# Performance work log

Measured on AMD Instinct MI355X. Metric: run time of the kernel, lower is better.

## Reference

```python
import jax, jax.numpy as jnp
import numpy as np

D_MODEL = 1024
N_HEADS = 16
D_HEAD = D_MODEL // N_HEADS
D_FF = 4096
ACT_BITS = 8
GSIZE = 64
EPS = 1e-6


def act_quant(x):
    # per-group int8 activation quantization with straight-through estimator
    qmax = 2.0 ** (ACT_BITS - 1) - 1.0  # 127
    g = x.reshape(x.shape[:-1] + (-1, GSIZE))
    s = jnp.clip(jnp.max(jnp.abs(g), axis=-1, keepdims=True), 1e-5, None) / qmax
    q = jnp.clip(jnp.round(g / s), -qmax, qmax) * s
    out = g + jax.lax.stop_gradient(q - g)  # STE
    return out.reshape(x.shape)


def weight_quant_1b(w):
    # binarize to sign(w) * mean(|w|), STE
    alpha = jnp.mean(jnp.abs(w))
    wq = jnp.sign(w) * alpha
    return w + jax.lax.stop_gradient(wq - w)


def bitlinear(x, w):
    # y = Q_act(x) @ Q_w(w)^T ; w is [out, in]
    return act_quant(x) @ weight_quant_1b(w).T


def rmsnorm(x, g):
    return x * jax.lax.rsqrt(jnp.mean(x * x, axis=-1, keepdims=True) + EPS) * g


def causal_sdpa(q, k, v):
    # q,k,v: [B,H,T,Dh]
    T = q.shape[2]
    scores = jnp.einsum('bhqd,bhkd->bhqk', q, k) / jnp.sqrt(jnp.asarray(D_HEAD, q.dtype))
    mask = jnp.tril(jnp.ones((T, T), dtype=bool))
    scores = jnp.where(mask, scores, jnp.asarray(-1e30, q.dtype))
    p = jax.nn.softmax(scores, axis=-1)
    return jnp.einsum('bhqk,bhkd->bhqd', p, v)


def setup_inputs() -> dict:
    key = jax.random.key(0)
    ks = jax.random.split(key, 11)
    sd = 0.02
    inp = {
        'x': jax.random.normal(ks[0], (1, 4096, D_MODEL), dtype=jnp.float32),
        'wq': jax.random.normal(ks[1], (D_MODEL, D_MODEL), dtype=jnp.float32) * sd,
        'wk': jax.random.normal(ks[2], (D_MODEL, D_MODEL), dtype=jnp.float32) * sd,
        'wv': jax.random.normal(ks[3], (D_MODEL, D_MODEL), dtype=jnp.float32) * sd,
        'wo': jax.random.normal(ks[4], (D_MODEL, D_MODEL), dtype=jnp.float32) * sd,
        'w1': jax.random.normal(ks[5], (D_FF, D_MODEL), dtype=jnp.float32) * sd,
        'w2': jax.random.normal(ks[6], (D_FF, D_MODEL), dtype=jnp.float32) * sd,
        'w3': jax.random.normal(ks[7], (D_MODEL, D_FF), dtype=jnp.float32) * sd,
        'g1': jnp.ones((D_MODEL,), dtype=jnp.float32),
        'g2': jnp.ones((D_MODEL,), dtype=jnp.float32),
    }
    return inp


def reference(x, wq, wk, wv, wo, w1, w2, w3, g1, g2):
    B, T, C = x.shape
    # attention branch
    h = rmsnorm(x, g1)
    q = bitlinear(h, wq).reshape(B, T, N_HEADS, D_HEAD).transpose(0, 2, 1, 3)
    k = bitlinear(h, wk).reshape(B, T, N_HEADS, D_HEAD).transpose(0, 2, 1, 3)
    v = bitlinear(h, wv).reshape(B, T, N_HEADS, D_HEAD).transpose(0, 2, 1, 3)
    y = causal_sdpa(q, k, v).transpose(0, 2, 1, 3).reshape(B, T, C)
    x = x + bitlinear(y, wo)
    # SwiGLU FFN branch
    h2 = rmsnorm(x, g2)
    ff = bitlinear(jax.nn.silu(bitlinear(h2, w1)) * bitlinear(h2, w2), w3)
    return x + ff
```

## Files before the change

### kernel.cpp

```cpp
#include <hip/hip_runtime.h>
#include <math.h>


typedef unsigned short u16;
typedef unsigned int u32;
typedef __attribute__((ext_vector_type(2))) unsigned int u32x2;
typedef __attribute__((ext_vector_type(4))) float f32x4;
typedef __attribute__((ext_vector_type(4))) unsigned short u16x4;
typedef __attribute__((ext_vector_type(8))) unsigned short u16x8;
typedef __attribute__((ext_vector_type(8))) __bf16 bf16x8;

#define DEV static __device__ __forceinline__

DEV float bf2f(u16 u) { union { unsigned i; float f; } c; c.i = ((unsigned)u) << 16; return c.f; }
DEV u16 f2bf(float f) { __bf16 b = (__bf16)f; return __builtin_bit_cast(u16, b); }
DEV float fexp2(float x) { float r; asm("v_exp_f32 %0, %1" : "=v"(r) : "v"(x)); return r; }
DEV u32 cvtpk(float lo, float hi) {
  u32 r; asm("v_cvt_pk_bf16_f32 %0, %1, %2" : "=v"(r) : "v"(lo), "v"(hi)); return r;
}

DEV void gload16(const void* g, void* l) {
  __builtin_amdgcn_global_load_lds((__attribute__((address_space(1))) void*)g,
                                   (__attribute__((address_space(3))) void*)l,
                                   16, 0, 0);
}

__global__ __launch_bounds__(256) void convert_sign_all(
    const float* __restrict__ w0, const float* __restrict__ w1,
    const float* __restrict__ w2, const float* __restrict__ w3,
    const float* __restrict__ w4, const float* __restrict__ w5,
    const float* __restrict__ w6, u16* __restrict__ sgn_base,
    float* __restrict__ partial,
    const float* __restrict__ x, const float* __restrict__ g1,
    u16* __restrict__ hq) {
  __shared__ float red[4];
  const int wi = blockIdx.y;
  const int t = threadIdx.x;

  if (wi == 7) {
#pragma unroll 1
    for (int rr = 0; rr < 16; ++rr) {
      const int row = blockIdx.x * 16 + rr;
      f32x4 v = ((const f32x4*)(x + (size_t)row * 1024))[t];
      float ss = v[0] * v[0] + v[1] * v[1] + v[2] * v[2] + v[3] * v[3];
#pragma unroll
      for (int off = 32; off >= 1; off >>= 1) ss += __shfl_xor(ss, off);
      if ((t & 63) == 0) red[t >> 6] = ss;
      __syncthreads();
      float tot = red[0] + red[1] + red[2] + red[3];
      __syncthreads();
      float rinv = rsqrtf(tot * (1.f / 1024.f) + 1e-6f);
      f32x4 gg = ((const f32x4*)g1)[t];
      float n[4];
#pragma unroll
      for (int j = 0; j < 4; ++j) n[j] = v[j] * rinv * gg[j];
      float gm = fmaxf(fmaxf(fabsf(n[0]), fabsf(n[1])), fmaxf(fabsf(n[2]), fabsf(n[3])));
#pragma unroll
      for (int off = 1; off <= 8; off <<= 1) gm = fmaxf(gm, __shfl_xor(gm, off));
      float s = fmaxf(gm, 1e-5f) / 127.0f;
      u16x4 o;
#pragma unroll
      for (int j = 0; j < 4; ++j) {
        float q = fminf(fmaxf(rintf(n[j] / s), -127.f), 127.f) * s;
        o[j] = f2bf(q);
      }
      ((u16x4*)hq)[(size_t)row * 256 + t] = o;
    }
    return;
  }

  const float* srcs[7] = {w0, w1, w2, w3, w4, w5, w6};
  const size_t offs[7] = {0, 1048576, 2097152, 3145728, 4194304, 4194304, 12582912};
  const float* w = srcs[wi];
  u16* sgn = sgn_base + offs[wi];
  const int n4 = (wi < 4) ? 262144 : 1048576;
  const bool ilv = (wi == 4) || (wi == 5);
  const int ilv_add = (wi == 5) ? 16 : 0;

  float s = 0.f;
  for (int i = blockIdx.x * 256 + t; i < n4; i += 256 * 256) {
    f32x4 v = ((const f32x4*)w)[i];
    u16x4 o;
#pragma unroll
    for (int j = 0; j < 4; ++j) {
      float f = v[j];
      o[j] = f > 0.f ? (u16)0x3F80 : (f < 0.f ? (u16)0xBF80 : (u16)0);
      s += fabsf(f);
    }
    size_t di = i;
    if (ilv) {
      int e = i << 2;
      int row = e >> 10, col = e & 1023;
      int dst = ((row >> 4) << 5) + ilv_add + (row & 15);
      di = ((size_t)dst << 8) + (col >> 2);
    }
    ((u16x4*)sgn)[di] = o;
  }
#pragma unroll
  for (int off = 32; off >= 1; off >>= 1) s += __shfl_xor(s, off);
  if ((t & 63) == 0) red[t >> 6] = s;
  __syncthreads();
  if (t == 0)
    partial[wi * 256 + blockIdx.x] = red[0] + red[1] + red[2] + red[3];
}

__global__ __launch_bounds__(256) void finalize_alpha(
    const float* __restrict__ partial, float* __restrict__ alphas) {
  __shared__ float red[4];
  int wi = blockIdx.x;
  float v = partial[wi * 256 + threadIdx.x];
#pragma unroll
  for (int off = 32; off >= 1; off >>= 1) v += __shfl_xor(v, off);
  if ((threadIdx.x & 63) == 0) red[threadIdx.x >> 6] = v;
  __syncthreads();
  if (threadIdx.x == 0)
    alphas[wi] = (red[0] + red[1] + red[2] + red[3]) *
                 (wi < 4 ? (1.f / 1048576.f) : (1.f / 4194304.f));
}

__global__ __launch_bounds__(256) void rmsnorm_quant(
    const float* __restrict__ x, const float* __restrict__ g, u16* __restrict__ out) {
  __shared__ float red[4];
  const int row = blockIdx.x, t = threadIdx.x;
  f32x4 v = ((const f32x4*)(x + (size_t)row * 1024))[t];
  float ss = v[0] * v[0] + v[1] * v[1] + v[2] * v[2] + v[3] * v[3];
#pragma unroll
  for (int off = 32; off >= 1; off >>= 1) ss += __shfl_xor(ss, off);
  if ((t & 63) == 0) red[t >> 6] = ss;
  __syncthreads();
  float tot = red[0] + red[1] + red[2] + red[3];
  float rinv = rsqrtf(tot * (1.f / 1024.f) + 1e-6f);
  f32x4 gg = ((const f32x4*)g)[t];
  float n[4];
#pragma unroll
  for (int j = 0; j < 4; ++j) n[j] = v[j] * rinv * gg[j];
  float gm = fmaxf(fmaxf(fabsf(n[0]), fabsf(n[1])), fmaxf(fabsf(n[2]), fabsf(n[3])));
#pragma unroll
  for (int off = 1; off <= 8; off <<= 1) gm = fmaxf(gm, __shfl_xor(gm, off));
  float s = fmaxf(gm, 1e-5f) / 127.0f;
  u16x4 o;
#pragma unroll
  for (int j = 0; j < 4; ++j) {
    float q = fminf(fmaxf(rintf(n[j] / s), -127.f), 127.f) * s;
    o[j] = f2bf(q);
  }
  ((u16x4*)out)[(size_t)row * 256 + t] = o;
}

__global__ __launch_bounds__(256) void transpose_v(
    const u16* __restrict__ qkv, u16* __restrict__ Vt) {
  __shared__ u16 T[64][65];
  const int tt = blockIdx.x, h = blockIdx.y, tid = threadIdx.x;
#pragma unroll
  for (int i = 0; i < 2; ++i) {
    int idx = i * 2048 + tid * 8;
    int trow = idx >> 6, dcol = idx & 63;
    u16x8 v = *(const u16x8*)(qkv + (size_t)(tt * 64 + trow) * 3072 + 2048 + h * 64 + dcol);
#pragma unroll
    for (int j = 0; j < 8; ++j) T[dcol + j][trow] = v[j];
  }
  __syncthreads();
#pragma unroll
  for (int i = 0; i < 2; ++i) {
    int idx = i * 2048 + tid * 8;
    int drow = idx >> 6, tcol = idx & 63;
    u16x8 v;
#pragma unroll
    for (int j = 0; j < 8; ++j) v[j] = T[drow][tcol + j];
    *(u16x8*)(Vt + ((size_t)h * 64 + drow) * 4096 + tt * 64 + tcol) = v;
  }
}

template <bool RES, int BM>
__global__ __launch_bounds__(256) void gemm_bt(
    const u16* __restrict__ A, const u16* __restrict__ B,
    const float* __restrict__ alpha, int ashift, const float* __restrict__ res,
    void* __restrict__ Cout, int M, int N, int K) {
  constexpr int NI = (BM == 128) ? 4 : 2;
  constexpr int WNE = (BM == 128) ? 64 : 32;
  __shared__ u16 As[BM * 64];
  __shared__ u16 Bs[128 * 64];
  const int tid = threadIdx.x;
  const int l = tid & 63, w = tid >> 6;
  const int wm = (BM == 128) ? (w >> 1) : 0;
  const int wn = (BM == 128) ? (w & 1) : w;
  const int lr = l & 15, lg = l >> 4;
  const int xorv = (l & 7) << 4;
  const int brow = blockIdx.y * BM;
  const int bcol = blockIdx.x * 128;
  const int src_chunk = (l & 7) ^ (l >> 3);
  const int rl = w * 8 + (l >> 3);

  f32x4 acc[4][NI];
#pragma unroll
  for (int i = 0; i < 4; ++i)
#pragma unroll
    for (int j = 0; j < NI; ++j) acc[i][j] = (f32x4){0.f, 0.f, 0.f, 0.f};

  const char* Ag = (const char*)A;
  const char* Bg = (const char*)B;
  const int nkt = K >> 6;
  for (int kt = 0; kt < nkt; ++kt) {
    __syncthreads();
    const size_t kb = (size_t)kt * 128 + src_chunk * 16;
#pragma unroll
    for (int it = 0; it < BM / 32; ++it)
      gload16(Ag + (size_t)(brow + it * 32 + rl) * (size_t)(K * 2) + kb,
              &As[(it * 32 + w * 8) * 64]);
#pragma unroll
    for (int it = 0; it < 4; ++it)
      gload16(Bg + (size_t)(bcol + it * 32 + rl) * (size_t)(K * 2) + kb,
              &Bs[(it * 32 + w * 8) * 64]);
    __syncthreads();

    bf16x8 af[4][2], bfr[NI][2];
#pragma unroll
    for (int mi = 0; mi < 4; ++mi)
#pragma unroll
      for (int ks = 0; ks < 2; ++ks) {
        int row = wm * 64 + mi * 16 + lr;
        af[mi][ks] = *(const bf16x8*)((const char*)As + row * 128 + ((ks * 64 + lg * 16) ^ xorv));
      }
#pragma unroll
    for (int ni = 0; ni < NI; ++ni)
#pragma unroll
      for (int ks = 0; ks < 2; ++ks) {
        int row = wn * WNE + ni * 16 + lr;
        bfr[ni][ks] = *(const bf16x8*)((const char*)Bs + row * 128 + ((ks * 64 + lg * 16) ^ xorv));
      }
#pragma unroll
    for (int ks = 0; ks < 2; ++ks)
#pragma unroll
      for (int mi = 0; mi < 4; ++mi)
#pragma unroll
        for (int ni = 0; ni < NI; ++ni)
          acc[mi][ni] = __builtin_amdgcn_mfma_f32_16x16x32_bf16(
              af[mi][ks], bfr[ni][ks], acc[mi][ni], 0, 0, 0);
  }

  const float scale = alpha[bcol >> ashift];
#pragma unroll
  for (int mi = 0; mi < 4; ++mi)
#pragma unroll
    for (int ni = 0; ni < NI; ++ni)
#pragma unroll
      for (int r = 0; r < 4; ++r) {
        int row = brow + wm * 64 + mi * 16 + lg * 4 + r;
        int col = bcol + wn * WNE + ni * 16 + lr;
        float vv = acc[mi][ni][r] * scale;
        if (RES)
          ((float*)Cout)[(size_t)row * N + col] = res[(size_t)row * N + col] + vv;
        else
          ((u16*)Cout)[(size_t)row * N + col] = f2bf(vv);
      }
}

template <bool RES>
__global__ __launch_bounds__(256, 2) void gemm_fat(
    const u16* __restrict__ A, const u16* __restrict__ B,
    const float* __restrict__ alpha, int ashift, const float* __restrict__ res,
    void* __restrict__ Cout, int M, int N, int K) {
  __shared__ u16 As[256 * 64];
  __shared__ u16 Bs[128 * 64];
  const int tid = threadIdx.x;
  const int l = tid & 63, w = tid >> 6;
  const int wm = w >> 1, wn = w & 1;
  const int lr = l & 15, lg = l >> 4;
  const int xorv = (l & 7) << 4;
  const int brow = blockIdx.y * 256;
  const int bcol = blockIdx.x * 128;
  const int src_chunk = (l & 7) ^ (l >> 3);
  const int rl = w * 8 + (l >> 3);

  f32x4 acc[8][4];
#pragma unroll
  for (int i = 0; i < 8; ++i)
#pragma unroll
    for (int j = 0; j < 4; ++j) acc[i][j] = (f32x4){0.f, 0.f, 0.f, 0.f};

  const int nkt = K >> 6;
  for (int kt = 0; kt < nkt; ++kt) {
    __syncthreads();
    const size_t kb = (size_t)kt * 128 + src_chunk * 16;
#pragma unroll
    for (int it = 0; it < 8; ++it)
      gload16((const char*)A + (size_t)(brow + it * 32 + rl) * (size_t)(K * 2) + kb,
              &As[(it * 32 + w * 8) * 64]);
#pragma unroll
    for (int it = 0; it < 4; ++it)
      gload16((const char*)B + (size_t)(bcol + it * 32 + rl) * (size_t)(K * 2) + kb,
              &Bs[(it * 32 + w * 8) * 64]);
    __syncthreads();

#pragma unroll
    for (int ks = 0; ks < 2; ++ks) {
      bf16x8 bfr[4];
#pragma unroll
      for (int ni = 0; ni < 4; ++ni)
        bfr[ni] = *(const bf16x8*)((const char*)Bs + (wn * 64 + ni * 16 + lr) * 128 +
                                   ((ks * 64 + lg * 16) ^ xorv));
#pragma unroll
      for (int mi = 0; mi < 8; ++mi) {
        bf16x8 af = *(const bf16x8*)((const char*)As + (wm * 128 + mi * 16 + lr) * 128 +
                                     ((ks * 64 + lg * 16) ^ xorv));
#pragma unroll
        for (int ni = 0; ni < 4; ++ni)
          acc[mi][ni] = __builtin_amdgcn_mfma_f32_16x16x32_bf16(
              af, bfr[ni], acc[mi][ni], 0, 0, 0);
      }
    }
  }

  const float scale = alpha[bcol >> ashift];
#pragma unroll
  for (int mi = 0; mi < 8; ++mi)
#pragma unroll
    for (int ni = 0; ni < 4; ++ni)
#pragma unroll
      for (int r = 0; r < 4; ++r) {
        int row = brow + wm * 128 + mi * 16 + lg * 4 + r;
        int col = bcol + wn * 64 + ni * 16 + lr;
        float vv = acc[mi][ni][r] * scale;
        if (RES)
          ((float*)Cout)[(size_t)row * N + col] = res[(size_t)row * N + col] + vv;
        else
          ((u16*)Cout)[(size_t)row * N + col] = f2bf(vv);
      }
}

__global__ __launch_bounds__(256, 2) void gemm_ffn(
    const u16* __restrict__ A, const u16* __restrict__ B12,
    const float* __restrict__ alpha2, u16* __restrict__ zq) {
  __shared__ u16 As[256 * 64];
  __shared__ u16 Bs[128 * 64];
  const int tid = threadIdx.x;
  const int l = tid & 63, w = tid >> 6;
  const int wm = w >> 1, wn = w & 1;
  const int lr = l & 15, lg = l >> 4;
  const int xorv = (l & 7) << 4;
  const int brow = blockIdx.y * 256;
  const int bcol = blockIdx.x * 128;
  const int src_chunk = (l & 7) ^ (l >> 3);
  const int rl = w * 8 + (l >> 3);

  f32x4 acc[8][4];
#pragma unroll
  for (int i = 0; i < 8; ++i)
#pragma unroll
    for (int j = 0; j < 4; ++j) acc[i][j] = (f32x4){0.f, 0.f, 0.f, 0.f};

  for (int kt = 0; kt < 16; ++kt) {
    __syncthreads();
    const size_t kb = (size_t)kt * 128 + src_chunk * 16;
#pragma unroll
    for (int it = 0; it < 8; ++it)
      gload16((const char*)A + (size_t)(brow + it * 32 + rl) * 2048 + kb,
              &As[(it * 32 + w * 8) * 64]);
#pragma unroll
    for (int it = 0; it < 4; ++it)
      gload16((const char*)B12 + (size_t)(bcol + it * 32 + rl) * 2048 + kb,
              &Bs[(it * 32 + w * 8) * 64]);
    __syncthreads();

#pragma unroll
    for (int ks = 0; ks < 2; ++ks) {
      bf16x8 bfr[4];
#pragma unroll
      for (int ni = 0; ni < 4; ++ni)
        bfr[ni] = *(const bf16x8*)((const char*)Bs + (wn * 64 + ni * 16 + lr) * 128 +
                                   ((ks * 64 + lg * 16) ^ xorv));
#pragma unroll
      for (int mi = 0; mi < 8; ++mi) {
        bf16x8 af = *(const bf16x8*)((const char*)As + (wm * 128 + mi * 16 + lr) * 128 +
                                     ((ks * 64 + lg * 16) ^ xorv));
#pragma unroll
        for (int ni = 0; ni < 4; ++ni)
          acc[mi][ni] = __builtin_amdgcn_mfma_f32_16x16x32_bf16(
              af, bfr[ni], acc[mi][ni], 0, 0, 0);
      }
    }
  }

  const float a1 = alpha2[0], a2 = alpha2[1];
  const float L2E = 1.4426950408889634f;
  float zl[8][4], zh[8][4], rm[8][4];
#pragma unroll
  for (int mi = 0; mi < 8; ++mi)
#pragma unroll
    for (int r = 0; r < 4; ++r) {
      float y1 = acc[mi][0][r] * a1;
      zl[mi][r] = y1 / (1.f + fexp2(-L2E * y1)) * (acc[mi][1][r] * a2);
      float y3 = acc[mi][2][r] * a1;
      zh[mi][r] = y3 / (1.f + fexp2(-L2E * y3)) * (acc[mi][3][r] * a2);
      float g = fmaxf(fabsf(zl[mi][r]), fabsf(zh[mi][r]));
#pragma unroll
      for (int off = 1; off <= 8; off <<= 1) g = fmaxf(g, __shfl_xor(g, off));
      rm[mi][r] = g;
    }

  float* rmax = (float*)&As[0];
  __syncthreads();
  if (lr == 0) {
#pragma unroll
    for (int mi = 0; mi < 8; ++mi)
#pragma unroll
      for (int r = 0; r < 4; ++r)
        rmax[w * 128 + mi * 16 + lg * 4 + r] = rm[mi][r];
  }
  __syncthreads();

#pragma unroll
  for (int mi = 0; mi < 8; ++mi)
#pragma unroll
    for (int r = 0; r < 4; ++r) {
      float g = fmaxf(rm[mi][r], rmax[(w ^ 1) * 128 + mi * 16 + lg * 4 + r]);
      float gmc = fmaxf(g, 1e-5f);
      float s = gmc * (1.f / 127.f);
      float inv = 127.f / gmc;
      int row = brow + wm * 128 + mi * 16 + lg * 4 + r;
      int zc = blockIdx.x * 64 + wn * 32 + lr;
      float q0 = fminf(fmaxf(rintf(zl[mi][r] * inv), -127.f), 127.f) * s;
      float q1 = fminf(fmaxf(rintf(zh[mi][r] * inv), -127.f), 127.f) * s;
      zq[(size_t)row * 4096 + zc] = f2bf(q0);
      zq[(size_t)row * 4096 + zc + 16] = f2bf(q1);
    }
}

__global__ __launch_bounds__(512) void attn_kernel(
    const u16* __restrict__ QKV, const u16* __restrict__ Vt, u16* __restrict__ Y) {
  __shared__ u16 Ks[2][64 * 64];
  __shared__ u16 Vs[2][64 * 64];
  __shared__ u16 Ps[8][16 * 64];

  const int tid = threadIdx.x;
  const int l = tid & 63, w = tid >> 6;
  const int lr = l & 15, lg = l >> 4;
  const int xorv = (l & 7) << 4;
  const int h = blockIdx.x;
  const int y = blockIdx.y;
  const int qt = (y < 16) ? y : (47 - y);
  const int src_chunk = (l & 7) ^ (l >> 3);
  const int rl = w * 8 + (l >> 3);
  const float SC = 0.18033688f;

  const int qrow0 = qt * 128 + w * 16;
  const int nkt = 2 * qt + 2;

  bf16x8 qf[2];
#pragma unroll
  for (int ks = 0; ks < 2; ++ks)
    qf[ks] = __builtin_bit_cast(
        bf16x8, *(const u16x8*)(QKV + (size_t)(qrow0 + lr) * 3072 +
                                h * 64 + ks * 32 + lg * 8));

  f32x4 O[4];
#pragma unroll
  for (int ni = 0; ni < 4; ++ni) O[ni] = (f32x4){0.f, 0.f, 0.f, 0.f};
  float m_ = -3e38f, lsum = 0.f;

  auto STAGE = [&](int buf, int kt) {
    int krow = kt * 64 + rl;
    gload16((const char*)QKV + ((size_t)krow * 3072 + 1024 + h * 64) * 2 + src_chunk * 16,
            &Ks[buf][(w * 8) * 64]);
    gload16((const char*)Vt + (((size_t)h * 64 + rl) * 4096 + kt * 64) * 2 + src_chunk * 16,
            &Vs[buf][(w * 8) * 64]);
  };

  STAGE(0, 0);
#pragma unroll 1
  for (int kt = 0; kt < nkt; ++kt) {
    const int cur = kt & 1;
    if (kt + 1 < nkt) {
      STAGE(cur ^ 1, kt + 1);
      asm volatile("s_waitcnt vmcnt(2)" ::: "memory");
    } else {
      asm volatile("s_waitcnt vmcnt(0)" ::: "memory");
    }
    __builtin_amdgcn_s_barrier();
    __builtin_amdgcn_sched_barrier(0);

    const char* kbase = (const char*)&Ks[cur][0];
    const char* vbase = (const char*)&Vs[cur][0];

    f32x4 S[4];
    __builtin_amdgcn_s_setprio(1);
#pragma unroll
    for (int ni = 0; ni < 4; ++ni) {
      S[ni] = (f32x4){0.f, 0.f, 0.f, 0.f};
#pragma unroll
      for (int ks = 0; ks < 2; ++ks) {
        bf16x8 kf = *(const bf16x8*)(kbase + (ni * 16 + lr) * 128 +
                                     ((ks * 64 + lg * 16) ^ xorv));
        S[ni] = __builtin_amdgcn_mfma_f32_16x16x32_bf16(kf, qf[ks], S[ni], 0, 0, 0);
      }
    }
    __builtin_amdgcn_s_setprio(0);

    const int tb = kt * 64;
    if (tb + 63 > qrow0) {
#pragma unroll
      for (int ni = 0; ni < 4; ++ni)
#pragma unroll
        for (int r = 0; r < 4; ++r)
          if (tb + ni * 16 + lg * 4 + r > qrow0 + lr) S[ni][r] = -3e38f;
    }

    float nm = -3e38f;
#pragma unroll
    for (int ni = 0; ni < 4; ++ni)
#pragma unroll
      for (int r = 0; r < 4; ++r) nm = fmaxf(nm, S[ni][r]);
    nm = fmaxf(nm, __shfl_xor(nm, 16));
    nm = fmaxf(nm, __shfl_xor(nm, 32));
    float nms = nm * SC;
    if (__ballot(nms > m_ + 8.f)) {
      float mn = fmaxf(m_, nms);
      float fac = fexp2(m_ - mn);
      m_ = mn;
      lsum *= fac;
#pragma unroll
      for (int ni = 0; ni < 4; ++ni) O[ni] *= fac;
    }
    float rs = 0.f;
#pragma unroll
    for (int ni = 0; ni < 4; ++ni)
#pragma unroll
      for (int r = 0; r < 4; ++r) {
        float pv = fexp2(__builtin_fmaf(S[ni][r], SC, -m_));
        S[ni][r] = pv;
        rs += pv;
      }
    rs += __shfl_xor(rs, 16);
    rs += __shfl_xor(rs, 32);
    lsum += rs;

#pragma unroll
    for (int ni = 0; ni < 4; ++ni) {
      u32x2 pk;
      pk[0] = cvtpk(S[ni][0], S[ni][1]);
      pk[1] = cvtpk(S[ni][2], S[ni][3]);
      *(u32x2*)((char*)&Ps[w][0] + lr * 128 + ((ni * 32 + lg * 8) ^ xorv)) = pk;
    }
    bf16x8 pt[2];
#pragma unroll
    for (int ks = 0; ks < 2; ++ks)
      pt[ks] = *(const bf16x8*)((const char*)&Ps[w][0] + lr * 128 +
                                ((ks * 64 + lg * 16) ^ xorv));

    __builtin_amdgcn_s_setprio(1);
#pragma unroll
    for (int ni = 0; ni < 4; ++ni) {
#pragma unroll
      for (int ks = 0; ks < 2; ++ks) {
        bf16x8 vf = *(const bf16x8*)(vbase + (ni * 16 + lr) * 128 +
                                     ((ks * 64 + lg * 16) ^ xorv));
        O[ni] = __builtin_amdgcn_mfma_f32_16x16x32_bf16(vf, pt[ks], O[ni], 0, 0, 0);
      }
    }
    __builtin_amdgcn_s_setprio(0);
    asm volatile("" ::: "memory");
    __builtin_amdgcn_s_barrier();
  }

  float rinv = 1.f / lsum;
  float o[4][4];
  float gm = 0.f;
#pragma unroll
  for (int ni = 0; ni < 4; ++ni)
#pragma unroll
    for (int r = 0; r < 4; ++r) {
      o[ni][r] = O[ni][r] * rinv;
      gm = fmaxf(gm, fabsf(o[ni][r]));
    }
  gm = fmaxf(gm, __shfl_xor(gm, 16));
  gm = fmaxf(gm, __shfl_xor(gm, 32));
  float gmc = fmaxf(gm, 1e-5f);
  float s = gmc * (1.f / 127.f);
  float inv = 127.f / gmc;
#pragma unroll
  for (int ni = 0; ni < 4; ++ni) {
    u16x4 ov;
#pragma unroll
    for (int r = 0; r < 4; ++r) {
      float q = fminf(fmaxf(rintf(o[ni][r] * inv), -127.f), 127.f) * s;
      ov[r] = f2bf(q);
    }
    *(u16x4*)(Y + (size_t)(qrow0 + lr) * 1024 + h * 64 + ni * 16 + lg * 4) = ov;
  }
}

extern "C" void kernel_launch(void* const* d_in, const int* in_sizes, int n_in,
                              void* d_out, int out_size, void* d_ws, size_t ws_size,
                              hipStream_t stream) {
  const float* x  = (const float*)d_in[0];
  const float* wq = (const float*)d_in[1];
  const float* wk = (const float*)d_in[2];
  const float* wv = (const float*)d_in[3];
  const float* wo = (const float*)d_in[4];
  const float* w1 = (const float*)d_in[5];
  const float* w2 = (const float*)d_in[6];
  const float* w3 = (const float*)d_in[7];
  const float* g1 = (const float*)d_in[8];
  const float* g2 = (const float*)d_in[9];

  char* ws = (char*)d_ws;
  const size_t MB = 1024 * 1024;
  u16* sgn   = (u16*)ws;
  u16* sWq   = (u16*)(ws + 0 * MB);
  u16* sWo   = (u16*)(ws + 6 * MB);
  u16* sW12  = (u16*)(ws + 8 * MB);
  u16* sW3   = (u16*)(ws + 24 * MB);
  float* partial = (float*)(ws + 32 * MB);
  float* alphas  = (float*)(ws + 32 * MB + 16384);
  u16* Vt    = (u16*)(ws + 33 * MB);
  float* x1  = (float*)(ws + 33 * MB);
  u16* hq    = (u16*)(ws + 49 * MB);
  u16* qkv   = (u16*)(ws + 57 * MB);
  u16* yb    = (u16*)(ws + 81 * MB);
  u16* zq    = (u16*)(ws + 57 * MB);

  convert_sign_all<<<dim3(256, 8), 256, 0, stream>>>(wq, wk, wv, wo, w1, w2, w3,
                                                     sgn, partial, x, g1, hq);
  finalize_alpha<<<7, 256, 0, stream>>>(partial, alphas);

  gemm_fat<false><<<dim3(24, 16), 256, 0, stream>>>(hq, sWq, alphas, 10, nullptr,
                                                    qkv, 4096, 3072, 1024);
  transpose_v<<<dim3(64, 16), 256, 0, stream>>>(qkv, Vt);
  attn_kernel<<<dim3(16, 32), 512, 0, stream>>>(qkv, Vt, yb);
  gemm_bt<true, 64><<<dim3(8, 64), 256, 0, stream>>>(yb, sWo, alphas + 3, 31, x,
                                                     x1, 4096, 1024, 1024);
  rmsnorm_quant<<<4096, 256, 0, stream>>>(x1, g2, hq);
  gemm_ffn<<<dim3(64, 16), 256, 0, stream>>>(hq, sW12, alphas + 4, zq);
  gemm_bt<true, 64><<<dim3(8, 64), 256, 0, stream>>>(zq, sW3, alphas + 6, 31, x1,
                                                     (float*)d_out, 4096, 1024, 4096);
}
```

Measured before the change: 307.4 us.

## Load attention K/V fragments directly from global memory and halve query tile

The attention kernel no longer stages K and V tiles through double-buffered LDS with global_load_lds and block barriers. Each wave now loads its MFMA K and V fragments straight from global memory into registers. The query tile shrinks from 128 to 64 rows with 256-thread blocks, doubling the grid, and the causal pairing is adjusted to match. This removes LDS traffic and barriers and raises occupancy, but every wave re-reads the same K/V from global or cache, and there is no software prefetch to hide load latency.

Result: slower. 450.8 us (+46.6%).

```diff
diff --git a/kernel.cpp b/kernel.cpp
--- a/kernel.cpp
+++ b/kernel.cpp
@@ -18,6 +18,7 @@
 DEV u32 cvtpk(float lo, float hi) {
   u32 r; asm("v_cvt_pk_bf16_f32 %0, %1, %2" : "=v"(r) : "v"(lo), "v"(hi)); return r;
 }
+DEV bf16x8 ld8(const u16* p) { return __builtin_bit_cast(bf16x8, *(const u16x8*)p); }
 
 DEV void gload16(const void* g, void* l) {
   __builtin_amdgcn_global_load_lds((__attribute__((address_space(1))) void*)g,
@@ -426,11 +427,9 @@
     }
 }
 
-__global__ __launch_bounds__(512) void attn_kernel(
+__global__ __launch_bounds__(256, 4) void attn_kernel(
     const u16* __restrict__ QKV, const u16* __restrict__ Vt, u16* __restrict__ Y) {
-  __shared__ u16 Ks[2][64 * 64];
-  __shared__ u16 Vs[2][64 * 64];
-  __shared__ u16 Ps[8][16 * 64];
+  __shared__ u16 Ps[4][16 * 64];
 
   const int tid = threadIdx.x;
   const int l = tid & 63, w = tid >> 6;
@@ -438,49 +437,34 @@
   const int xorv = (l & 7) << 4;
   const int h = blockIdx.x;
   const int y = blockIdx.y;
-  const int qt = (y < 16) ? y : (47 - y);
-  const int src_chunk = (l & 7) ^ (l >> 3);
-  const int rl = w * 8 + (l >> 3);
+  const int qt = (y < 32) ? y : (95 - y);
   const float SC = 0.18033688f;
 
-  const int qrow0 = qt * 128 + w * 16;
-  const int nkt = 2 * qt + 2;
+  const int qrow0 = qt * 64 + w * 16;
+  const int nkt = qt + 1;
 
   bf16x8 qf[2];
 #pragma unroll
   for (int ks = 0; ks < 2; ++ks)
-    qf[ks] = __builtin_bit_cast(
-        bf16x8, *(const u16x8*)(QKV + (size_t)(qrow0 + lr) * 3072 +
-                                h * 64 + ks * 32 + lg * 8));
+    qf[ks] = ld8(QKV + (size_t)(qrow0 + lr) * 3072 + h * 64 + ks * 32 + lg * 8);
+
+  const u16* Kb = QKV + 1024 + h * 64 + (size_t)lr * 3072 + lg * 8;
+  const u16* Vb = Vt + ((size_t)(h * 64 + lr)) * 4096 + lg * 8;
 
   f32x4 O[4];
 #pragma unroll
   for (int ni = 0; ni < 4; ++ni) O[ni] = (f32x4){0.f, 0.f, 0.f, 0.f};
   float m_ = -3e38f, lsum = 0.f;
 
-  auto STAGE = [&](int buf, int kt) {
-    int krow = kt * 64 + rl;
-    gload16((const char*)QKV + ((size_t)krow * 3072 + 1024 + h * 64) * 2 + src_chunk * 16,
-            &Ks[buf][(w * 8) * 64]);
-    gload16((const char*)Vt + (((size_t)h * 64 + rl) * 4096 + kt * 64) * 2 + src_chunk * 16,
-            &Vs[buf][(w * 8) * 64]);
-  };
-
-  STAGE(0, 0);
 #pragma unroll 1
   for (int kt = 0; kt < nkt; ++kt) {
-    const int cur = kt & 1;
-    if (kt + 1 < nkt) {
-      STAGE(cur ^ 1, kt + 1);
-      asm volatile("s_waitcnt vmcnt(2)" ::: "memory");
-    } else {
-      asm volatile("s_waitcnt vmcnt(0)" ::: "memory");
-    }
-    __builtin_amdgcn_s_barrier();
-    __builtin_amdgcn_sched_barrier(0);
-
-    const char* kbase = (const char*)&Ks[cur][0];
-    const char* vbase = (const char*)&Vs[cur][0];
+    const u16* kp = Kb + (size_t)(kt * 64) * 3072;
+    bf16x8 kf[4][2];
+#pragma unroll
+    for (int ni = 0; ni < 4; ++ni)
+#pragma unroll
+      for (int ks = 0; ks < 2; ++ks)
+        kf[ni][ks] = ld8(kp + (size_t)(ni * 16) * 3072 + ks * 32);
 
     f32x4 S[4];
     __builtin_amdgcn_s_setprio(1);
@@ -488,13 +472,18 @@
     for (int ni = 0; ni < 4; ++ni) {
       S[ni] = (f32x4){0.f, 0.f, 0.f, 0.f};
 #pragma unroll
-      for (int ks = 0; ks < 2; ++ks) {
-        bf16x8 kf = *(const bf16x8*)(kbase + (ni * 16 + lr) * 128 +
-                                     ((ks * 64 + lg * 16) ^ xorv));
-        S[ni] = __builtin_amdgcn_mfma_f32_16x16x32_bf16(kf, qf[ks], S[ni], 0, 0, 0);
-      }
+      for (int ks = 0; ks < 2; ++ks)
+        S[ni] = __builtin_amdgcn_mfma_f32_16x16x32_bf16(kf[ni][ks], qf[ks], S[ni], 0, 0, 0);
     }
     __builtin_amdgcn_s_setprio(0);
+
+    const u16* vp = Vb + kt * 64;
+    bf16x8 vf[4][2];
+#pragma unroll
+    for (int ni = 0; ni < 4; ++ni)
+#pragma unroll
+      for (int ks = 0; ks < 2; ++ks)
+        vf[ni][ks] = ld8(vp + (size_t)(ni * 16) * 4096 + ks * 32);
 
     const int tb = kt * 64;
     if (tb + 63 > qrow0) {
@@ -549,17 +538,11 @@
 
     __builtin_amdgcn_s_setprio(1);
 #pragma unroll
-    for (int ni = 0; ni < 4; ++ni) {
-#pragma unroll
-      for (int ks = 0; ks < 2; ++ks) {
-        bf16x8 vf = *(const bf16x8*)(vbase + (ni * 16 + lr) * 128 +
-                                     ((ks * 64 + lg * 16) ^ xorv));
-        O[ni] = __builtin_amdgcn_mfma_f32_16x16x32_bf16(vf, pt[ks], O[ni], 0, 0, 0);
-      }
-    }
+    for (int ni = 0; ni < 4; ++ni)
+#pragma unroll
+      for (int ks = 0; ks < 2; ++ks)
+        O[ni] = __builtin_amdgcn_mfma_f32_16x16x32_bf16(vf[ni][ks], pt[ks], O[ni], 0, 0, 0);
     __builtin_amdgcn_s_setprio(0);
-    asm volatile("" ::: "memory");
-    __builtin_amdgcn_s_barrier();
   }
 
   float rinv = 1.f / lsum;
@@ -626,7 +609,7 @@
   gemm_fat<false><<<dim3(24, 16), 256, 0, stream>>>(hq, sWq, alphas, 10, nullptr,
                                                     qkv, 4096, 3072, 1024);
   transpose_v<<<dim3(64, 16), 256, 0, stream>>>(qkv, Vt);
-  attn_kernel<<<dim3(16, 32), 512, 0, stream>>>(qkv, Vt, yb);
+  attn_kernel<<<dim3(16, 64), 256, 0, stream>>>(qkv, Vt, yb);
   gemm_bt<true, 64><<<dim3(8, 64), 256, 0, stream>>>(yb, sWo, alphas + 3, 31, x,
                                                      x1, 4096, 1024, 1024);
   rmsnorm_quant<<<4096, 256, 0, stream>>>(x1, g2, hq);
```

## Give each attention wave private K/V tiles and drop block barriers

Applied to the files above, without the earlier changes.

The attention kernel changes from 512-thread blocks with a 128-row query tile to 256-thread blocks with a 64-row query tile, using a grid twice as large. Each wave now stages its own 32-key K/V tiles into private LDS buffers, so the per-iteration block barriers go away and each wave's causal trip count stops at its own diagonal. This removes barrier stalls and skips fully masked key tiles per wave. In exchange, every wave loads K/V from global memory separately, so there is no sharing within a block and global/L2 traffic goes up, and the narrower 32-key steps double the number of softmax iterations.

Result: slower. 371.1 us (+20.7%).

```diff
diff --git a/kernel.cpp b/kernel.cpp
--- a/kernel.cpp
+++ b/kernel.cpp
@@ -426,25 +426,25 @@
     }
 }
 
-__global__ __launch_bounds__(512) void attn_kernel(
+__global__ __launch_bounds__(256) void attn_kernel(
     const u16* __restrict__ QKV, const u16* __restrict__ Vt, u16* __restrict__ Y) {
-  __shared__ u16 Ks[2][64 * 64];
-  __shared__ u16 Vs[2][64 * 64];
-  __shared__ u16 Ps[8][16 * 64];
+  __shared__ u16 Ks[4][2][32 * 64];
+  __shared__ u16 Vs[4][2][64 * 32];
+  __shared__ u16 Ps[4][16 * 32];
 
   const int tid = threadIdx.x;
   const int l = tid & 63, w = tid >> 6;
   const int lr = l & 15, lg = l >> 4;
-  const int xorv = (l & 7) << 4;
   const int h = blockIdx.x;
   const int y = blockIdx.y;
-  const int qt = (y < 16) ? y : (47 - y);
-  const int src_chunk = (l & 7) ^ (l >> 3);
-  const int rl = w * 8 + (l >> 3);
+  const int qt = (y < 32) ? y : (95 - y);
   const float SC = 0.18033688f;
 
-  const int qrow0 = qt * 128 + w * 16;
-  const int nkt = 2 * qt + 2;
+  const int qrow0 = qt * 64 + w * 16;
+  const int nkt = 2 * qt + 1 + (w >> 1);
+
+  const int kchunk = (l & 7) ^ (l >> 3);
+  const int vchunk = (l & 3) ^ ((l >> 2) & 3);
 
   bf16x8 qf[2];
 #pragma unroll
@@ -459,11 +459,18 @@
   float m_ = -3e38f, lsum = 0.f;
 
   auto STAGE = [&](int buf, int kt) {
-    int krow = kt * 64 + rl;
-    gload16((const char*)QKV + ((size_t)krow * 3072 + 1024 + h * 64) * 2 + src_chunk * 16,
-            &Ks[buf][(w * 8) * 64]);
-    gload16((const char*)Vt + (((size_t)h * 64 + rl) * 4096 + kt * 64) * 2 + src_chunk * 16,
-            &Vs[buf][(w * 8) * 64]);
+#pragma unroll
+    for (int it = 0; it < 4; ++it) {
+      int krow = kt * 32 + it * 8 + (l >> 3);
+      gload16((const char*)QKV + ((size_t)krow * 3072 + 1024 + h * 64) * 2 + kchunk * 16,
+              &Ks[w][buf][(it * 8) * 64]);
+    }
+#pragma unroll
+    for (int it = 0; it < 4; ++it) {
+      int drow = it * 16 + (l >> 2);
+      gload16((const char*)Vt + (((size_t)h * 64 + drow) * 4096 + kt * 32) * 2 + vchunk * 16,
+              &Vs[w][buf][(it * 16) * 32]);
+    }
   };
 
   STAGE(0, 0);
@@ -472,44 +479,46 @@
     const int cur = kt & 1;
     if (kt + 1 < nkt) {
       STAGE(cur ^ 1, kt + 1);
-      asm volatile("s_waitcnt vmcnt(2)" ::: "memory");
+      asm volatile("s_waitcnt vmcnt(8)" ::: "memory");
     } else {
       asm volatile("s_waitcnt vmcnt(0)" ::: "memory");
     }
-    __builtin_amdgcn_s_barrier();
     __builtin_amdgcn_sched_barrier(0);
 
-    const char* kbase = (const char*)&Ks[cur][0];
-    const char* vbase = (const char*)&Vs[cur][0];
-
-    f32x4 S[4];
+    const char* kbase = (const char*)&Ks[w][cur][0];
+    const char* vbase = (const char*)&Vs[w][cur][0];
+
+    f32x4 S[2];
     __builtin_amdgcn_s_setprio(1);
 #pragma unroll
-    for (int ni = 0; ni < 4; ++ni) {
+    for (int ni = 0; ni < 2; ++ni) {
       S[ni] = (f32x4){0.f, 0.f, 0.f, 0.f};
 #pragma unroll
       for (int ks = 0; ks < 2; ++ks) {
         bf16x8 kf = *(const bf16x8*)(kbase + (ni * 16 + lr) * 128 +
-                                     ((ks * 64 + lg * 16) ^ xorv));
+                                     ((ks * 64 + lg * 16) ^ ((lr & 7) << 4)));
         S[ni] = __builtin_amdgcn_mfma_f32_16x16x32_bf16(kf, qf[ks], S[ni], 0, 0, 0);
       }
     }
     __builtin_amdgcn_s_setprio(0);
 
-    const int tb = kt * 64;
-    if (tb + 63 > qrow0) {
-#pragma unroll
-      for (int ni = 0; ni < 4; ++ni)
+    bf16x8 vf[4];
+#pragma unroll
+    for (int ni = 0; ni < 4; ++ni)
+      vf[ni] = *(const bf16x8*)(vbase + (ni * 16 + lr) * 64 +
+                                ((lg * 16) ^ ((lr & 3) << 4)));
+
+    const int tb = kt * 32;
+    if (tb + 31 > qrow0) {
+#pragma unroll
+      for (int ni = 0; ni < 2; ++ni)
 #pragma unroll
         for (int r = 0; r < 4; ++r)
           if (tb + ni * 16 + lg * 4 + r > qrow0 + lr) S[ni][r] = -3e38f;
     }
 
-    float nm = -3e38f;
-#pragma unroll
-    for (int ni = 0; ni < 4; ++ni)
-#pragma unroll
-      for (int r = 0; r < 4; ++r) nm = fmaxf(nm, S[ni][r]);
+    float nm = fmaxf(fmaxf(S[0][0], S[0][1]), fmaxf(S[0][2], S[0][3]));
+    nm = fmaxf(nm, fmaxf(fmaxf(S[1][0], S[1][1]), fmaxf(S[1][2], S[1][3])));
     nm = fmaxf(nm, __shfl_xor(nm, 16));
     nm = fmaxf(nm, __shfl_xor(nm, 32));
     float nms = nm * SC;
@@ -523,7 +532,7 @@
     }
     float rs = 0.f;
 #pragma unroll
-    for (int ni = 0; ni < 4; ++ni)
+    for (int ni = 0; ni < 2; ++ni)
 #pragma unroll
       for (int r = 0; r < 4; ++r) {
         float pv = fexp2(__builtin_fmaf(S[ni][r], SC, -m_));
@@ -535,31 +544,20 @@
     lsum += rs;
 
 #pragma unroll
-    for (int ni = 0; ni < 4; ++ni) {
+    for (int ni = 0; ni < 2; ++ni) {
       u32x2 pk;
       pk[0] = cvtpk(S[ni][0], S[ni][1]);
       pk[1] = cvtpk(S[ni][2], S[ni][3]);
-      *(u32x2*)((char*)&Ps[w][0] + lr * 128 + ((ni * 32 + lg * 8) ^ xorv)) = pk;
-    }
-    bf16x8 pt[2];
-#pragma unroll
-    for (int ks = 0; ks < 2; ++ks)
-      pt[ks] = *(const bf16x8*)((const char*)&Ps[w][0] + lr * 128 +
-                                ((ks * 64 + lg * 16) ^ xorv));
+      *(u32x2*)((char*)&Ps[w][0] + lr * 64 + ((ni * 32 + lg * 8) ^ ((lr & 3) << 4))) = pk;
+    }
+    bf16x8 pt = *(const bf16x8*)((const char*)&Ps[w][0] + lr * 64 +
+                                 ((lg * 16) ^ ((lr & 3) << 4)));
 
     __builtin_amdgcn_s_setprio(1);
 #pragma unroll
-    for (int ni = 0; ni < 4; ++ni) {
-#pragma unroll
-      for (int ks = 0; ks < 2; ++ks) {
-        bf16x8 vf = *(const bf16x8*)(vbase + (ni * 16 + lr) * 128 +
-                                     ((ks * 64 + lg * 16) ^ xorv));
-        O[ni] = __builtin_amdgcn_mfma_f32_16x16x32_bf16(vf, pt[ks], O[ni], 0, 0, 0);
-      }
-    }
+    for (int ni = 0; ni < 4; ++ni)
+      O[ni] = __builtin_amdgcn_mfma_f32_16x16x32_bf16(vf[ni], pt, O[ni], 0, 0, 0);
     __builtin_amdgcn_s_setprio(0);
-    asm volatile("" ::: "memory");
-    __builtin_amdgcn_s_barrier();
   }
 
   float rinv = 1.f / lsum;
@@ -626,7 +624,7 @@
   gemm_fat<false><<<dim3(24, 16), 256, 0, stream>>>(hq, sWq, alphas, 10, nullptr,
                                                     qkv, 4096, 3072, 1024);
   transpose_v<<<dim3(64, 16), 256, 0, stream>>>(qkv, Vt);
-  attn_kernel<<<dim3(16, 32), 512, 0, stream>>>(qkv, Vt, yb);
+  attn_kernel<<<dim3(16, 64), 256, 0, stream>>>(qkv, Vt, yb);
   gemm_bt<true, 64><<<dim3(8, 64), 256, 0, stream>>>(yb, sWo, alphas + 3, 31, x,
                                                      x1, 4096, 1024, 1024);
   rmsnorm_quant<<<4096, 256, 0, stream>>>(x1, g2, hq);
```

## Give each attention wave two 16-row query tiles and halve the block size

Applied to the files above, without the earlier changes.

The attention kernel now runs 4 waves per block instead of 8, with each wave handling 32 query rows (two 16-row m-tiles) rather than 16. Each K and V fragment read from LDS is reused for two MFMAs, which halves LDS read traffic per unit of compute, and staging now issues two loads per thread per tile. The cost is doubled accumulator and score registers per wave, with possible occupancy loss. There are also fewer waves per block to hide latency.

Measured after the change: 333.0 us. +8.3%, slower.

```diff
diff --git a/kernel.cpp b/kernel.cpp
--- a/kernel.cpp
+++ b/kernel.cpp
@@ -426,11 +426,11 @@
     }
 }
 
-__global__ __launch_bounds__(512) void attn_kernel(
+__global__ __launch_bounds__(256) void attn_kernel(
     const u16* __restrict__ QKV, const u16* __restrict__ Vt, u16* __restrict__ Y) {
   __shared__ u16 Ks[2][64 * 64];
   __shared__ u16 Vs[2][64 * 64];
-  __shared__ u16 Ps[8][16 * 64];
+  __shared__ u16 Ps[4][32 * 64];
 
   const int tid = threadIdx.x;
   const int l = tid & 63, w = tid >> 6;
@@ -443,27 +443,35 @@
   const int rl = w * 8 + (l >> 3);
   const float SC = 0.18033688f;
 
-  const int qrow0 = qt * 128 + w * 16;
+  const int qrow0 = qt * 128 + w * 32;
   const int nkt = 2 * qt + 2;
 
-  bf16x8 qf[2];
-#pragma unroll
-  for (int ks = 0; ks < 2; ++ks)
-    qf[ks] = __builtin_bit_cast(
-        bf16x8, *(const u16x8*)(QKV + (size_t)(qrow0 + lr) * 3072 +
-                                h * 64 + ks * 32 + lg * 8));
-
-  f32x4 O[4];
-#pragma unroll
-  for (int ni = 0; ni < 4; ++ni) O[ni] = (f32x4){0.f, 0.f, 0.f, 0.f};
-  float m_ = -3e38f, lsum = 0.f;
+  bf16x8 qf[2][2];
+#pragma unroll
+  for (int mi = 0; mi < 2; ++mi)
+#pragma unroll
+    for (int ks = 0; ks < 2; ++ks)
+      qf[mi][ks] = __builtin_bit_cast(
+          bf16x8, *(const u16x8*)(QKV + (size_t)(qrow0 + mi * 16 + lr) * 3072 +
+                                  h * 64 + ks * 32 + lg * 8));
+
+  f32x4 O[2][4];
+#pragma unroll
+  for (int mi = 0; mi < 2; ++mi)
+#pragma unroll
+    for (int ni = 0; ni < 4; ++ni) O[mi][ni] = (f32x4){0.f, 0.f, 0.f, 0.f};
+  float m_[2] = {-3e38f, -3e38f}, lsum[2] = {0.f, 0.f};
 
   auto STAGE = [&](int buf, int kt) {
-    int krow = kt * 64 + rl;
-    gload16((const char*)QKV + ((size_t)krow * 3072 + 1024 + h * 64) * 2 + src_chunk * 16,
-            &Ks[buf][(w * 8) * 64]);
-    gload16((const char*)Vt + (((size_t)h * 64 + rl) * 4096 + kt * 64) * 2 + src_chunk * 16,
-            &Vs[buf][(w * 8) * 64]);
+#pragma unroll
+    for (int it = 0; it < 2; ++it) {
+      int krow = kt * 64 + it * 32 + rl;
+      gload16((const char*)QKV + ((size_t)krow * 3072 + 1024 + h * 64) * 2 + src_chunk * 16,
+              &Ks[buf][(it * 32 + w * 8) * 64]);
+      int drow = it * 32 + rl;
+      gload16((const char*)Vt + (((size_t)h * 64 + drow) * 4096 + kt * 64) * 2 + src_chunk * 16,
+              &Vs[buf][(it * 32 + w * 8) * 64]);
+    }
   };
 
   STAGE(0, 0);
@@ -472,7 +480,7 @@
     const int cur = kt & 1;
     if (kt + 1 < nkt) {
       STAGE(cur ^ 1, kt + 1);
-      asm volatile("s_waitcnt vmcnt(2)" ::: "memory");
+      asm volatile("s_waitcnt vmcnt(4)" ::: "memory");
     } else {
       asm volatile("s_waitcnt vmcnt(0)" ::: "memory");
     }
@@ -482,16 +490,22 @@
     const char* kbase = (const char*)&Ks[cur][0];
     const char* vbase = (const char*)&Vs[cur][0];
 
-    f32x4 S[4];
+    f32x4 S[2][4];
     __builtin_amdgcn_s_setprio(1);
 #pragma unroll
     for (int ni = 0; ni < 4; ++ni) {
-      S[ni] = (f32x4){0.f, 0.f, 0.f, 0.f};
-#pragma unroll
-      for (int ks = 0; ks < 2; ++ks) {
-        bf16x8 kf = *(const bf16x8*)(kbase + (ni * 16 + lr) * 128 +
-                                     ((ks * 64 + lg * 16) ^ xorv));
-        S[ni] = __builtin_amdgcn_mfma_f32_16x16x32_bf16(kf, qf[ks], S[ni], 0, 0, 0);
+      bf16x8 kf[2];
+#pragma unroll
+      for (int ks = 0; ks < 2; ++ks)
+        kf[ks] = *(const bf16x8*)(kbase + (ni * 16 + lr) * 128 +
+                                  ((ks * 64 + lg * 16) ^ xorv));
+#pragma unroll
+      for (int mi = 0; mi < 2; ++mi) {
+        S[mi][ni] = (f32x4){0.f, 0.f, 0.f, 0.f};
+#pragma unroll
+        for (int ks = 0; ks < 2; ++ks)
+          S[mi][ni] = __builtin_amdgcn_mfma_f32_16x16x32_bf16(kf[ks], qf[mi][ks],
+                                                              S[mi][ni], 0, 0, 0);
       }
     }
     __builtin_amdgcn_s_setprio(0);
@@ -499,93 +513,111 @@
     const int tb = kt * 64;
     if (tb + 63 > qrow0) {
 #pragma unroll
+      for (int mi = 0; mi < 2; ++mi)
+#pragma unroll
+        for (int ni = 0; ni < 4; ++ni)
+#pragma unroll
+          for (int r = 0; r < 4; ++r)
+            if (tb + ni * 16 + lg * 4 + r > qrow0 + mi * 16 + lr) S[mi][ni][r] = -3e38f;
+    }
+
+#pragma unroll
+    for (int mi = 0; mi < 2; ++mi) {
+      float nm = -3e38f;
+#pragma unroll
       for (int ni = 0; ni < 4; ++ni)
 #pragma unroll
-        for (int r = 0; r < 4; ++r)
-          if (tb + ni * 16 + lg * 4 + r > qrow0 + lr) S[ni][r] = -3e38f;
-    }
-
-    float nm = -3e38f;
-#pragma unroll
-    for (int ni = 0; ni < 4; ++ni)
-#pragma unroll
-      for (int r = 0; r < 4; ++r) nm = fmaxf(nm, S[ni][r]);
-    nm = fmaxf(nm, __shfl_xor(nm, 16));
-    nm = fmaxf(nm, __shfl_xor(nm, 32));
-    float nms = nm * SC;
-    if (__ballot(nms > m_ + 8.f)) {
-      float mn = fmaxf(m_, nms);
-      float fac = fexp2(m_ - mn);
-      m_ = mn;
-      lsum *= fac;
-#pragma unroll
-      for (int ni = 0; ni < 4; ++ni) O[ni] *= fac;
-    }
-    float rs = 0.f;
-#pragma unroll
-    for (int ni = 0; ni < 4; ++ni)
-#pragma unroll
-      for (int r = 0; r < 4; ++r) {
-        float pv = fexp2(__builtin_fmaf(S[ni][r], SC, -m_));
-        S[ni][r] = pv;
-        rs += pv;
-      }
-    rs += __shfl_xor(rs, 16);
-    rs += __shfl_xor(rs, 32);
-    lsum += rs;
-
+        for (int r = 0; r < 4; ++r) nm = fmaxf(nm, S[mi][ni][r]);
+      nm = fmaxf(nm, __shfl_xor(nm, 16));
+      nm = fmaxf(nm, __shfl_xor(nm, 32));
+      float nms = nm * SC;
+      if (__ballot(nms > m_[mi] + 8.f)) {
+        float mn = fmaxf(m_[mi], nms);
+        float fac = fexp2(m_[mi] - mn);
+        m_[mi] = mn;
+        lsum[mi] *= fac;
+#pragma unroll
+        for (int ni = 0; ni < 4; ++ni) O[mi][ni] *= fac;
+      }
+      float rs = 0.f;
+#pragma unroll
+      for (int ni = 0; ni < 4; ++ni)
+#pragma unroll
+        for (int r = 0; r < 4; ++r) {
+          float pv = fexp2(__builtin_fmaf(S[mi][ni][r], SC, -m_[mi]));
+          S[mi][ni][r] = pv;
+          rs += pv;
+        }
+      rs += __shfl_xor(rs, 16);
+      rs += __shfl_xor(rs, 32);
+      lsum[mi] += rs;
+    }
+
+#pragma unroll
+    for (int mi = 0; mi < 2; ++mi)
+#pragma unroll
+      for (int ni = 0; ni < 4; ++ni) {
+        u32x2 pk;
+        pk[0] = cvtpk(S[mi][ni][0], S[mi][ni][1]);
+        pk[1] = cvtpk(S[mi][ni][2], S[mi][ni][3]);
+        *(u32x2*)((char*)&Ps[w][0] + (mi * 16 + lr) * 128 +
+                  ((ni * 32 + lg * 8) ^ xorv)) = pk;
+      }
+    bf16x8 pt[2][2];
+#pragma unroll
+    for (int mi = 0; mi < 2; ++mi)
+#pragma unroll
+      for (int ks = 0; ks < 2; ++ks)
+        pt[mi][ks] = *(const bf16x8*)((const char*)&Ps[w][0] + (mi * 16 + lr) * 128 +
+                                      ((ks * 64 + lg * 16) ^ xorv));
+
+    __builtin_amdgcn_s_setprio(1);
 #pragma unroll
     for (int ni = 0; ni < 4; ++ni) {
-      u32x2 pk;
-      pk[0] = cvtpk(S[ni][0], S[ni][1]);
-      pk[1] = cvtpk(S[ni][2], S[ni][3]);
-      *(u32x2*)((char*)&Ps[w][0] + lr * 128 + ((ni * 32 + lg * 8) ^ xorv)) = pk;
-    }
-    bf16x8 pt[2];
-#pragma unroll
-    for (int ks = 0; ks < 2; ++ks)
-      pt[ks] = *(const bf16x8*)((const char*)&Ps[w][0] + lr * 128 +
-                                ((ks * 64 + lg * 16) ^ xorv));
-
-    __builtin_amdgcn_s_setprio(1);
-#pragma unroll
-    for (int ni = 0; ni < 4; ++ni) {
-#pragma unroll
-      for (int ks = 0; ks < 2; ++ks) {
-        bf16x8 vf = *(const bf16x8*)(vbase + (ni * 16 + lr) * 128 +
-                                     ((ks * 64 + lg * 16) ^ xorv));
-        O[ni] = __builtin_amdgcn_mfma_f32_16x16x32_bf16(vf, pt[ks], O[ni], 0, 0, 0);
-      }
+      bf16x8 vf[2];
+#pragma unroll
+      for (int ks = 0; ks < 2; ++ks)
+        vf[ks] = *(const bf16x8*)(vbase + (ni * 16 + lr) * 128 +
+                                  ((ks * 64 + lg * 16) ^ xorv));
+#pragma unroll
+      for (int mi = 0; mi < 2; ++mi)
+#pragma unroll
+        for (int ks = 0; ks < 2; ++ks)
+          O[mi][ni] = __builtin_amdgcn_mfma_f32_16x16x32_bf16(vf[ks], pt[mi][ks],
+                                                              O[mi][ni], 0, 0, 0);
     }
     __builtin_amdgcn_s_setprio(0);
     asm volatile("" ::: "memory");
     __builtin_amdgcn_s_barrier();
   }
 
-  float rinv = 1.f / lsum;
-  float o[4][4];
-  float gm = 0.f;
-#pragma unroll
-  for (int ni = 0; ni < 4; ++ni)
-#pragma unroll
-    for (int r = 0; r < 4; ++r) {
-      o[ni][r] = O[ni][r] * rinv;
-      gm = fmaxf(gm, fabsf(o[ni][r]));
-    }
-  gm = fmaxf(gm, __shfl_xor(gm, 16));
-  gm = fmaxf(gm, __shfl_xor(gm, 32));
-  float gmc = fmaxf(gm, 1e-5f);
-  float s = gmc * (1.f / 127.f);
-  float inv = 127.f / gmc;
-#pragma unroll
-  for (int ni = 0; ni < 4; ++ni) {
-    u16x4 ov;
-#pragma unroll
-    for (int r = 0; r < 4; ++r) {
-      float q = fminf(fmaxf(rintf(o[ni][r] * inv), -127.f), 127.f) * s;
-      ov[r] = f2bf(q);
-    }
-    *(u16x4*)(Y + (size_t)(qrow0 + lr) * 1024 + h * 64 + ni * 16 + lg * 4) = ov;
+#pragma unroll
+  for (int mi = 0; mi < 2; ++mi) {
+    float rinv = 1.f / lsum[mi];
+    float o[4][4];
+    float gm = 0.f;
+#pragma unroll
+    for (int ni = 0; ni < 4; ++ni)
+#pragma unroll
+      for (int r = 0; r < 4; ++r) {
+        o[ni][r] = O[mi][ni][r] * rinv;
+        gm = fmaxf(gm, fabsf(o[ni][r]));
+      }
+    gm = fmaxf(gm, __shfl_xor(gm, 16));
+    gm = fmaxf(gm, __shfl_xor(gm, 32));
+    float gmc = fmaxf(gm, 1e-5f);
+    float s = gmc * (1.f / 127.f);
+    float inv = 127.f / gmc;
+#pragma unroll
+    for (int ni = 0; ni < 4; ++ni) {
+      u16x4 ov;
+#pragma unroll
+      for (int r = 0; r < 4; ++r) {
+        float q = fminf(fmaxf(rintf(o[ni][r] * inv), -127.f), 127.f) * s;
+        ov[r] = f2bf(q);
+      }
+      *(u16x4*)(Y + (size_t)(qrow0 + mi * 16 + lr) * 1024 + h * 64 + ni * 16 + lg * 4) = ov;
+    }
   }
 }
 
@@ -626,7 +658,7 @@
   gemm_fat<false><<<dim3(24, 16), 256, 0, stream>>>(hq, sWq, alphas, 10, nullptr,
                                                     qkv, 4096, 3072, 1024);
   transpose_v<<<dim3(64, 16), 256, 0, stream>>>(qkv, Vt);
-  attn_kernel<<<dim3(16, 32), 512, 0, stream>>>(qkv, Vt, yb);
+  attn_kernel<<<dim3(16, 32), 256, 0, stream>>>(qkv, Vt, yb);
   gemm_bt<true, 64><<<dim3(8, 64), 256, 0, stream>>>(yb, sWo, alphas + 3, 31, x,
                                                      x1, 4096, 1024, 1024);
   rmsnorm_quant<<<4096, 256, 0, stream>>>(x1, g2, hq);
```
